# Optimization experiments

Hardware: AMD Instinct MI355X
Metric: run time of the kernel (lower is better)

The kernel has to match this reference:

```python
import jax, jax.numpy as jnp
import numpy as np

N = 8192      # number of graph nodes
C = 256       # feature_size
D = C // 2    # projection dim


def setup_inputs() -> dict:
    key = jax.random.key(0)
    ks = jax.random.split(key, 10)
    s_in = 1.0 / np.sqrt(C + 3)   # torch Linear default init scale (uniform bound)
    s_r = 1.0 / np.sqrt(D)
    return {
        "landmarks": jax.random.normal(ks[0], (1, N, 3), dtype=jnp.float32),
        "features": jax.random.normal(ks[1], (1, N, C), dtype=jnp.float32),
        # weights stored [in, out]
        "Wi": jax.random.uniform(ks[2], (C + 3, D), jnp.float32, -s_in, s_in),
        "bi": jax.random.uniform(ks[3], (D,), jnp.float32, -s_in, s_in),
        "Wj": jax.random.uniform(ks[4], (C + 3, D), jnp.float32, -s_in, s_in),
        "bj": jax.random.uniform(ks[5], (D,), jnp.float32, -s_in, s_in),
        "Wk": jax.random.uniform(ks[6], (C + 3, D), jnp.float32, -s_in, s_in),
        "bk": jax.random.uniform(ks[7], (D,), jnp.float32, -s_in, s_in),
        "Wr": jax.random.uniform(ks[8], (D, C), jnp.float32, -s_r, s_r),
        "br": jax.random.uniform(ks[9], (C,), jnp.float32, -s_r, s_r),
    }


def reference(landmarks, features, Wi, bi, Wj, bj, Wk, bk, Wr, br):
    # concat coords + features, drop the singleton batch dim: [N, C+3]
    x = jnp.concatenate([landmarks, features], axis=2)[0]
    fi = x @ Wi + bi                       # [N, D]
    fj = x @ Wj + bj                       # [N, D]
    fk = x @ Wk + bk                       # [N, D]
    att = jax.nn.sigmoid(fi @ fj.T)        # [N, N] sigmoid scores (non-softmax)
    att = att / jnp.sum(att, axis=1, keepdims=True)  # row-sum normalize
    out = (att @ fk) @ Wr + br             # [N, C] restored
    return features + out[None]            # residual, back to [1, N, C]
```

## Files before the change

kernel.cpp:

```cpp
#include <hip/hip_runtime.h>
#include <stdint.h>

#define N_NODES 8192
#define KPAD 272
#define OUTC 384

typedef __attribute__((ext_vector_type(8))) short bhalf8;
typedef __attribute__((ext_vector_type(16))) float f32x16;
typedef __attribute__((ext_vector_type(4))) float f32x4;

__device__ inline unsigned short f2bf_rne(float f) {
    unsigned u = __builtin_bit_cast(unsigned, f);
    u += 0x7FFFu + ((u >> 16) & 1u);
    return (unsigned short)(u >> 16);
}

__device__ inline bhalf8 mk8(unsigned a, unsigned b, unsigned c, unsigned d) {
    union { unsigned u[4]; bhalf8 v; } U;
    U.u[0] = a; U.u[1] = b; U.u[2] = c; U.u[3] = d;
    return U.v;
}

#define GLD_TO_LDS(gptr, lptr)                                                              \
    __builtin_amdgcn_global_load_lds((const __attribute__((address_space(1))) void*)(gptr), \
                                     (__attribute__((address_space(3))) void*)(lptr), 16, 0, 0)

__global__ void k_prep(const float* __restrict__ landmarks, const float* __restrict__ features,
                       const float* __restrict__ Wi, const float* __restrict__ bi,
                       const float* __restrict__ Wj, const float* __restrict__ bj,
                       const float* __restrict__ Wk, const float* __restrict__ bk,
                       const float* __restrict__ Wr,
                       unsigned short* __restrict__ xb, unsigned short* __restrict__ WcatT,
                       unsigned short* __restrict__ WrT, float* __restrict__ bcat) {
    int idx = blockIdx.x * 256 + threadIdx.x;
    const int XB_N = N_NODES * KPAD;
    const int WC_N = OUTC * KPAD;
    const int WR_N = 256 * 128;
    if (idx < XB_N) {
        int i = idx / KPAD, kk = idx - i * KPAD;
        float v = 0.f;
        if (kk < 256) v = features[i * 256 + kk];
        else if (kk < 259) v = landmarks[i * 3 + (kk - 256)];
        xb[idx] = f2bf_rne(v);
        return;
    }
    idx -= XB_N;
    if (idx < WC_N) {
        int n = idx / KPAD, kk = idx - n * KPAD;
        int sel = n >> 7, d = n & 127;
        const float* W = (sel == 0) ? Wi : ((sel == 1) ? Wj : Wk);
        float v = 0.f;
        if (kk < 256) v = W[(kk + 3) * 128 + d];
        else if (kk < 259) v = W[(kk - 256) * 128 + d];
        WcatT[idx] = f2bf_rne(v);
        return;
    }
    idx -= WC_N;
    if (idx < WR_N) {
        int c = idx >> 7, d = idx & 127;
        WrT[idx] = f2bf_rne(Wr[d * 256 + c]);
        return;
    }
    idx -= WR_N;
    if (idx < OUTC) {
        float v = (idx < 128) ? bi[idx] : ((idx < 256) ? bj[idx - 128] : bk[idx - 256]);
        bcat[idx] = v;
    }
}

__global__ __launch_bounds__(256) void k_proj(const unsigned short* __restrict__ xb,
                                              const unsigned short* __restrict__ WcatT,
                                              const float* __restrict__ bcat,
                                              unsigned short* __restrict__ fi,
                                              unsigned short* __restrict__ fj,
                                              unsigned short* __restrict__ fkT) {
    const int tid = threadIdx.x;
    const int w = tid >> 6, l = tid & 63, h = l >> 5, ln = l & 31;
    const int i0 = blockIdx.x * 32;
    f32x16 acc[3] = {};
#pragma unroll
    for (int s = 0; s < 17; ++s) {
        bhalf8 a = *(const bhalf8*)(xb + (size_t)(i0 + ln) * KPAD + s * 16 + h * 8);
#pragma unroll
        for (int t = 0; t < 3; ++t) {
            int n = 96 * w + 32 * t + ln;
            bhalf8 b = *(const bhalf8*)(WcatT + (size_t)n * KPAD + s * 16 + h * 8);
            acc[t] = __builtin_amdgcn_mfma_f32_32x32x16_bf16(a, b, acc[t], 0, 0, 0);
        }
    }
#pragma unroll
    for (int t = 0; t < 3; ++t) {
        int n = 96 * w + 32 * t + ln;
        int sel = n >> 7, d = n & 127;
        float bias = bcat[n];
#pragma unroll
        for (int q = 0; q < 4; ++q) {
            int ib = i0 + 8 * q + 4 * h;
            if (sel < 2) {
                unsigned short* dst = sel ? fj : fi;
#pragma unroll
                for (int r = 0; r < 4; ++r)
                    dst[(size_t)(ib + r) * 128 + d] = f2bf_rne(acc[t][4 * q + r] + bias);
            } else {
                ushort4 pk;
                pk.x = f2bf_rne(acc[t][4 * q + 0] + bias);
                pk.y = f2bf_rne(acc[t][4 * q + 1] + bias);
                pk.z = f2bf_rne(acc[t][4 * q + 2] + bias);
                pk.w = f2bf_rne(acc[t][4 * q + 3] + bias);
                *(ushort4*)(fkT + (size_t)d * N_NODES + ib) = pk;
            }
        }
    }
}

__global__ __launch_bounds__(256, 2) void k_attn(const unsigned short* __restrict__ fi,
                                                 const unsigned short* __restrict__ fj,
                                                 const unsigned short* __restrict__ fkT,
                                                 float* __restrict__ num_part,
                                                 float* __restrict__ den_part) {
    __shared__ __align__(16) char smem[65536];
    unsigned short* fj_s = (unsigned short*)smem;
    unsigned short* fk_s = (unsigned short*)(smem + 32768);
    float* bufA = (float*)smem;
    float* bufB = (float*)(smem + 17408);
    float* denb = (float*)(smem + 34816);

    const int tid = threadIdx.x;
    const int w = tid >> 6, l = tid & 63, h = l >> 5, ln = l & 31;
    const int rt = blockIdx.x & 127, jq = blockIdx.x >> 7;
    const int i0 = rt * 64;
    const int jbase = jq * 2048;

    bhalf8 bfi[2][8];
#pragma unroll
    for (int nt = 0; nt < 2; ++nt)
#pragma unroll
        for (int s = 0; s < 8; ++s)
            bfi[nt][s] = *(const bhalf8*)(fi + (size_t)(i0 + nt * 32 + ln) * 128 + s * 16 + h * 8);

    f32x16 acc[8] = {};
    float dacc0 = 0.f, dacc1 = 0.f;

    const int rsub = l >> 4;
    const int cph = l & 15;

    for (int mt = 0; mt < 16; ++mt) {
        const int j0 = jbase + mt * 128;
#pragma unroll
        for (int q = 0; q < 8; ++q) {
            int r = w * 32 + q * 4 + rsub;
            int c = cph ^ (r & 15);
            GLD_TO_LDS(fj + (size_t)(j0 + r) * 128 + c * 8, (char*)fj_s + (w * 32 + q * 4) * 256);
            GLD_TO_LDS(fkT + (size_t)r * N_NODES + j0 + c * 8, (char*)fk_s + (w * 32 + q * 4) * 256);
        }
        __syncthreads();

        f32x16 st0 = {}, st1 = {};
        const int jrow = w * 32 + ln;
#pragma unroll
        for (int s = 0; s < 8; ++s) {
            int c = (s * 2 + h) ^ (jrow & 15);
            bhalf8 af = *(const bhalf8*)((char*)fj_s + jrow * 256 + c * 16);
            st0 = __builtin_amdgcn_mfma_f32_32x32x16_bf16(af, bfi[0][s], st0, 0, 0, 0);
            st1 = __builtin_amdgcn_mfma_f32_32x32x16_bf16(af, bfi[1][s], st1, 0, 0, 0);
        }

        float sv0[16], sv1[16];
#pragma unroll
        for (int r = 0; r < 16; ++r) {
            float x0 = __builtin_amdgcn_rcpf(1.f + __builtin_amdgcn_exp2f(st0[r] * -1.44269504f));
            float x1 = __builtin_amdgcn_rcpf(1.f + __builtin_amdgcn_exp2f(st1[r] * -1.44269504f));
            dacc0 += x0; dacc1 += x1;
            sv0[r] = x0; sv1[r] = x1;
        }
        unsigned p0[8], p1[8], x0v[8], x1v[8];
#pragma unroll
        for (int q = 0; q < 8; ++q) {
            p0[q] = __builtin_amdgcn_perm(__builtin_bit_cast(unsigned, sv0[2 * q + 1]),
                                          __builtin_bit_cast(unsigned, sv0[2 * q]), 0x07060302u);
            p1[q] = __builtin_amdgcn_perm(__builtin_bit_cast(unsigned, sv1[2 * q + 1]),
                                          __builtin_bit_cast(unsigned, sv1[2 * q]), 0x07060302u);
        }
#pragma unroll
        for (int q = 0; q < 8; ++q) {
            x0v[q] = (unsigned)__shfl_xor((int)p0[q], 32, 64);
            x1v[q] = (unsigned)__shfl_xor((int)p1[q], 32, 64);
        }
        bhalf8 fb[2][2];
        if (h == 0) {
            fb[0][0] = mk8(p0[0], p0[1], x0v[0], x0v[1]);
            fb[0][1] = mk8(p0[4], p0[5], x0v[4], x0v[5]);
            fb[1][0] = mk8(p1[0], p1[1], x1v[0], x1v[1]);
            fb[1][1] = mk8(p1[4], p1[5], x1v[4], x1v[5]);
        } else {
            fb[0][0] = mk8(x0v[2], x0v[3], p0[2], p0[3]);
            fb[0][1] = mk8(x0v[6], x0v[7], p0[6], p0[7]);
            fb[1][0] = mk8(x1v[2], x1v[3], p1[2], p1[3]);
            fb[1][1] = mk8(x1v[6], x1v[7], p1[6], p1[7]);
        }
#pragma unroll
        for (int m4 = 0; m4 < 4; ++m4) {
#pragma unroll
            for (int s2 = 0; s2 < 2; ++s2) {
                int row = m4 * 32 + ln;
                int c = (w * 4 + s2 * 2 + h) ^ (row & 15);
                bhalf8 af = *(const bhalf8*)((char*)fk_s + row * 256 + c * 16);
                acc[m4 * 2 + 0] = __builtin_amdgcn_mfma_f32_32x32x16_bf16(af, fb[0][s2], acc[m4 * 2 + 0], 0, 0, 0);
                acc[m4 * 2 + 1] = __builtin_amdgcn_mfma_f32_32x32x16_bf16(af, fb[1][s2], acc[m4 * 2 + 1], 0, 0, 0);
            }
        }
        __syncthreads();
    }

    {
        float o0 = __shfl_xor(dacc0, 32, 64);
        float o1 = __shfl_xor(dacc1, 32, 64);
        dacc0 += o0; dacc1 += o1;
    }
    if (h == 0) {
        denb[w * 64 + ln] = dacc0;
        denb[w * 64 + 32 + ln] = dacc1;
    }

#pragma unroll
    for (int half = 0; half < 2; ++half) {
        __syncthreads();
        if (w < 2) {
            float* buf = w ? bufB : bufA;
#pragma unroll
            for (int m2 = 0; m2 < 2; ++m2) {
                int m4 = half * 2 + m2;
#pragma unroll
                for (int nt = 0; nt < 2; ++nt) {
                    int iloc = nt * 32 + ln;
#pragma unroll
                    for (int q = 0; q < 4; ++q) {
                        int d = m2 * 32 + 8 * q + 4 * h;
                        f32x4 v = {acc[m4 * 2 + nt][4 * q + 0], acc[m4 * 2 + nt][4 * q + 1],
                                   acc[m4 * 2 + nt][4 * q + 2], acc[m4 * 2 + nt][4 * q + 3]};
                        *(f32x4*)(buf + iloc * 68 + d) = v;
                    }
                }
            }
        }
        __syncthreads();
        if (w >= 2) {
            float* buf = (w == 3) ? bufB : bufA;
#pragma unroll
            for (int m2 = 0; m2 < 2; ++m2) {
                int m4 = half * 2 + m2;
#pragma unroll
                for (int nt = 0; nt < 2; ++nt) {
                    int iloc = nt * 32 + ln;
#pragma unroll
                    for (int q = 0; q < 4; ++q) {
                        int d = m2 * 32 + 8 * q + 4 * h;
                        f32x4 old = *(f32x4*)(buf + iloc * 68 + d);
                        f32x4 v = {acc[m4 * 2 + nt][4 * q + 0], acc[m4 * 2 + nt][4 * q + 1],
                                   acc[m4 * 2 + nt][4 * q + 2], acc[m4 * 2 + nt][4 * q + 3]};
                        *(f32x4*)(buf + iloc * 68 + d) = old + v;
                    }
                }
            }
        }
        __syncthreads();
#pragma unroll
        for (int e = 0; e < 4; ++e) {
            int v = e * 256 + tid;
            int iloc = v >> 4;
            int d4 = (v & 15) * 4;
            f32x4 s = *(f32x4*)(bufA + iloc * 68 + d4) + *(f32x4*)(bufB + iloc * 68 + d4);
            *(f32x4*)(num_part + (size_t)(jq * N_NODES + i0 + iloc) * 128 + half * 64 + d4) = s;
        }
    }
    __syncthreads();
    if (tid < 64) {
        den_part[(size_t)jq * N_NODES + i0 + tid] =
            denb[tid] + denb[64 + tid] + denb[128 + tid] + denb[192 + tid];
    }
}

__global__ void k_comb(const float* __restrict__ num_part, const float* __restrict__ den_part,
                       unsigned short* __restrict__ t) {
    int f = blockIdx.x * 256 + threadIdx.x;
    int i = f >> 5, d4 = (f & 31) * 4;
    f32x4 s = {};
    float ds = 0.f;
#pragma unroll
    for (int q = 0; q < 4; ++q) {
        s += *(const f32x4*)(num_part + (size_t)(q * N_NODES + i) * 128 + d4);
        ds += den_part[(size_t)q * N_NODES + i];
    }
    float inv = 1.0f / ds;
    ushort4 pk;
    pk.x = f2bf_rne(s.x * inv);
    pk.y = f2bf_rne(s.y * inv);
    pk.z = f2bf_rne(s.z * inv);
    pk.w = f2bf_rne(s.w * inv);
    *(ushort4*)(t + (size_t)i * 128 + d4) = pk;
}

__global__ __launch_bounds__(256) void k_out(const unsigned short* __restrict__ t,
                                             const unsigned short* __restrict__ WrT,
                                             const float* __restrict__ br,
                                             const float* __restrict__ features,
                                             float* __restrict__ out) {
    __shared__ __align__(16) char smem[65536];
    const int tid = threadIdx.x, w = tid >> 6, l = tid & 63, h = l >> 5, ln = l & 31;
    const int i0 = blockIdx.x * 32;
    {
        int rsub = l >> 4, cph = l & 15;
#pragma unroll
        for (int q = 0; q < 16; ++q) {
            int r = w * 64 + q * 4 + rsub;
            int c = cph ^ (r & 15);
            GLD_TO_LDS(WrT + (size_t)r * 128 + c * 8, (char*)smem + (w * 64 + q * 4) * 256);
        }
    }
    __syncthreads();
    f32x16 acc[2] = {};
#pragma unroll
    for (int s = 0; s < 8; ++s) {
        bhalf8 af = *(const bhalf8*)(t + (size_t)(i0 + ln) * 128 + s * 16 + h * 8);
#pragma unroll
        for (int nt = 0; nt < 2; ++nt) {
            int row = w * 64 + nt * 32 + ln;
            int c = (s * 2 + h) ^ (row & 15);
            bhalf8 bf = *(const bhalf8*)((char*)smem + row * 256 + c * 16);
            acc[nt] = __builtin_amdgcn_mfma_f32_32x32x16_bf16(af, bf, acc[nt], 0, 0, 0);
        }
    }
#pragma unroll
    for (int nt = 0; nt < 2; ++nt) {
        int cc = w * 64 + nt * 32 + ln;
        float bias = br[cc];
#pragma unroll
        for (int q = 0; q < 4; ++q) {
#pragma unroll
            for (int r = 0; r < 4; ++r) {
                int i = i0 + 8 * q + 4 * h + r;
                out[(size_t)i * 256 + cc] = acc[nt][4 * q + r] + bias + features[(size_t)i * 256 + cc];
            }
        }
    }
}

extern "C" void kernel_launch(void* const* d_in, const int* in_sizes, int n_in,
                              void* d_out, int out_size, void* d_ws, size_t ws_size,
                              hipStream_t stream) {
    const float* landmarks = (const float*)d_in[0];
    const float* features  = (const float*)d_in[1];
    const float* Wi = (const float*)d_in[2];
    const float* bi = (const float*)d_in[3];
    const float* Wj = (const float*)d_in[4];
    const float* bj = (const float*)d_in[5];
    const float* Wk = (const float*)d_in[6];
    const float* bk = (const float*)d_in[7];
    const float* Wr = (const float*)d_in[8];
    const float* br = (const float*)d_in[9];

    char* ws = (char*)d_ws;
    unsigned short* xb      = (unsigned short*)(ws + 0);
    unsigned short* WcatT   = (unsigned short*)(ws + 4456448);
    unsigned short* WrT     = (unsigned short*)(ws + 4665344);
    float*          bcat    = (float*)(ws + 4730880);
    unsigned short* fi      = (unsigned short*)(ws + 4732416);
    unsigned short* fjp     = (unsigned short*)(ws + 6829568);
    unsigned short* fkT     = (unsigned short*)(ws + 8926720);
    float*          num_part= (float*)(ws + 11023872);
    float*          den_part= (float*)(ws + 27801088);
    unsigned short* t       = (unsigned short*)(ws + 27932160);

    float* out = (float*)d_out;

    hipLaunchKernelGGL(k_prep, dim3(9242), dim3(256), 0, stream,
                       landmarks, features, Wi, bi, Wj, bj, Wk, bk, Wr, xb, WcatT, WrT, bcat);
    hipLaunchKernelGGL(k_proj, dim3(256), dim3(256), 0, stream, xb, WcatT, bcat, fi, fjp, fkT);
    hipLaunchKernelGGL(k_attn, dim3(512), dim3(256), 0, stream, fi, fjp, fkT, num_part, den_part);
    hipLaunchKernelGGL(k_comb, dim3(1024), dim3(256), 0, stream, num_part, den_part, t);
    hipLaunchKernelGGL(k_out, dim3(256), dim3(256), 0, stream, t, WrT, br, features, out);
}
```

Measured before the change: 183.5 us.

## Double-buffer attention tiles and split waves over i-halves and j-halves

Result: faster. 156.3 us (-14.8%).

```diff
diff --git a/kernel.cpp b/kernel.cpp
--- a/kernel.cpp
+++ b/kernel.cpp
@@ -119,164 +119,136 @@
                                                  float* __restrict__ num_part,
                                                  float* __restrict__ den_part) {
     __shared__ __align__(16) char smem[65536];
-    unsigned short* fj_s = (unsigned short*)smem;
-    unsigned short* fk_s = (unsigned short*)(smem + 32768);
-    float* bufA = (float*)smem;
-    float* bufB = (float*)(smem + 17408);
-    float* denb = (float*)(smem + 34816);
+    char* const fjb0 = smem;
+    char* const fkb0 = smem + 16384;
+    char* const fjb1 = smem + 32768;
+    char* const fkb1 = smem + 49152;
 
     const int tid = threadIdx.x;
     const int w = tid >> 6, l = tid & 63, h = l >> 5, ln = l & 31;
+    const int ih = w >> 1, jh = w & 1;
     const int rt = blockIdx.x & 127, jq = blockIdx.x >> 7;
     const int i0 = rt * 64;
     const int jbase = jq * 2048;
 
-    bhalf8 bfi[2][8];
-#pragma unroll
-    for (int nt = 0; nt < 2; ++nt)
-#pragma unroll
-        for (int s = 0; s < 8; ++s)
-            bfi[nt][s] = *(const bhalf8*)(fi + (size_t)(i0 + nt * 32 + ln) * 128 + s * 16 + h * 8);
-
-    f32x16 acc[8] = {};
-    float dacc0 = 0.f, dacc1 = 0.f;
-
-    const int rsub = l >> 4;
-    const int cph = l & 15;
-
-    for (int mt = 0; mt < 16; ++mt) {
-        const int j0 = jbase + mt * 128;
-#pragma unroll
-        for (int q = 0; q < 8; ++q) {
-            int r = w * 32 + q * 4 + rsub;
+    const int rsub = l >> 4, cph = l & 15;
+    const int rsub8 = l >> 3, cph8 = l & 7;
+
+    bhalf8 bfi[8];
+#pragma unroll
+    for (int s = 0; s < 8; ++s)
+        bfi[s] = *(const bhalf8*)(fi + (size_t)(i0 + ih * 32 + ln) * 128 + s * 16 + h * 8);
+
+    f32x16 acc[4] = {};
+    float dacc = 0.f;
+
+    auto STAGE = [&](char* fjd, char* fkd, int J0) {
+#pragma unroll
+        for (int q = 0; q < 4; ++q) {
+            int r = w * 16 + q * 4 + rsub;
             int c = cph ^ (r & 15);
-            GLD_TO_LDS(fj + (size_t)(j0 + r) * 128 + c * 8, (char*)fj_s + (w * 32 + q * 4) * 256);
-            GLD_TO_LDS(fkT + (size_t)r * N_NODES + j0 + c * 8, (char*)fk_s + (w * 32 + q * 4) * 256);
-        }
-        __syncthreads();
-
-        f32x16 st0 = {}, st1 = {};
-        const int jrow = w * 32 + ln;
+            GLD_TO_LDS(fj + (size_t)(J0 + r) * 128 + c * 8, fjd + (w * 16 + q * 4) * 256);
+        }
+#pragma unroll
+        for (int q = 0; q < 4; ++q) {
+            int r = w * 32 + q * 8 + rsub8;
+            int c = cph8 ^ (r & 7);
+            GLD_TO_LDS(fkT + (size_t)r * N_NODES + J0 + c * 8, fkd + (w * 32 + q * 8) * 128);
+        }
+    };
+
+    auto COMPUTE = [&](const char* fjbuf, const char* fkbuf) {
+        f32x16 st = {};
+        const int jrow = jh * 32 + ln;
 #pragma unroll
         for (int s = 0; s < 8; ++s) {
             int c = (s * 2 + h) ^ (jrow & 15);
-            bhalf8 af = *(const bhalf8*)((char*)fj_s + jrow * 256 + c * 16);
-            st0 = __builtin_amdgcn_mfma_f32_32x32x16_bf16(af, bfi[0][s], st0, 0, 0, 0);
-            st1 = __builtin_amdgcn_mfma_f32_32x32x16_bf16(af, bfi[1][s], st1, 0, 0, 0);
-        }
-
-        float sv0[16], sv1[16];
-#pragma unroll
-        for (int r = 0; r < 16; ++r) {
-            float x0 = __builtin_amdgcn_rcpf(1.f + __builtin_amdgcn_exp2f(st0[r] * -1.44269504f));
-            float x1 = __builtin_amdgcn_rcpf(1.f + __builtin_amdgcn_exp2f(st1[r] * -1.44269504f));
-            dacc0 += x0; dacc1 += x1;
-            sv0[r] = x0; sv1[r] = x1;
-        }
-        unsigned p0[8], p1[8], x0v[8], x1v[8];
+            bhalf8 af = *(const bhalf8*)(fjbuf + jrow * 256 + c * 16);
+            st = __builtin_amdgcn_mfma_f32_32x32x16_bf16(af, bfi[s], st, 0, 0, 0);
+        }
+        unsigned p[8], xw[8];
 #pragma unroll
         for (int q = 0; q < 8; ++q) {
-            p0[q] = __builtin_amdgcn_perm(__builtin_bit_cast(unsigned, sv0[2 * q + 1]),
-                                          __builtin_bit_cast(unsigned, sv0[2 * q]), 0x07060302u);
-            p1[q] = __builtin_amdgcn_perm(__builtin_bit_cast(unsigned, sv1[2 * q + 1]),
-                                          __builtin_bit_cast(unsigned, sv1[2 * q]), 0x07060302u);
-        }
-#pragma unroll
-        for (int q = 0; q < 8; ++q) {
-            x0v[q] = (unsigned)__shfl_xor((int)p0[q], 32, 64);
-            x1v[q] = (unsigned)__shfl_xor((int)p1[q], 32, 64);
-        }
-        bhalf8 fb[2][2];
+            float x0 = __builtin_amdgcn_rcpf(1.f + __builtin_amdgcn_exp2f(st[2 * q] * -1.44269504f));
+            float x1 = __builtin_amdgcn_rcpf(1.f + __builtin_amdgcn_exp2f(st[2 * q + 1] * -1.44269504f));
+            dacc += x0;
+            dacc += x1;
+            p[q] = __builtin_amdgcn_perm(__builtin_bit_cast(unsigned, x1),
+                                         __builtin_bit_cast(unsigned, x0), 0x07060302u);
+        }
+#pragma unroll
+        for (int q = 0; q < 8; ++q) xw[q] = (unsigned)__shfl_xor((int)p[q], 32, 64);
+        bhalf8 fb[2];
         if (h == 0) {
-            fb[0][0] = mk8(p0[0], p0[1], x0v[0], x0v[1]);
-            fb[0][1] = mk8(p0[4], p0[5], x0v[4], x0v[5]);
-            fb[1][0] = mk8(p1[0], p1[1], x1v[0], x1v[1]);
-            fb[1][1] = mk8(p1[4], p1[5], x1v[4], x1v[5]);
+            fb[0] = mk8(p[0], p[1], xw[0], xw[1]);
+            fb[1] = mk8(p[4], p[5], xw[4], xw[5]);
         } else {
-            fb[0][0] = mk8(x0v[2], x0v[3], p0[2], p0[3]);
-            fb[0][1] = mk8(x0v[6], x0v[7], p0[6], p0[7]);
-            fb[1][0] = mk8(x1v[2], x1v[3], p1[2], p1[3]);
-            fb[1][1] = mk8(x1v[6], x1v[7], p1[6], p1[7]);
+            fb[0] = mk8(xw[2], xw[3], p[2], p[3]);
+            fb[1] = mk8(xw[6], xw[7], p[6], p[7]);
         }
 #pragma unroll
         for (int m4 = 0; m4 < 4; ++m4) {
+            int row = m4 * 32 + ln;
 #pragma unroll
             for (int s2 = 0; s2 < 2; ++s2) {
-                int row = m4 * 32 + ln;
-                int c = (w * 4 + s2 * 2 + h) ^ (row & 15);
-                bhalf8 af = *(const bhalf8*)((char*)fk_s + row * 256 + c * 16);
-                acc[m4 * 2 + 0] = __builtin_amdgcn_mfma_f32_32x32x16_bf16(af, fb[0][s2], acc[m4 * 2 + 0], 0, 0, 0);
-                acc[m4 * 2 + 1] = __builtin_amdgcn_mfma_f32_32x32x16_bf16(af, fb[1][s2], acc[m4 * 2 + 1], 0, 0, 0);
-            }
-        }
+                int c = (jh * 4 + s2 * 2 + h) ^ (row & 7);
+                bhalf8 af = *(const bhalf8*)(fkbuf + row * 128 + c * 16);
+                acc[m4] = __builtin_amdgcn_mfma_f32_32x32x16_bf16(af, fb[s2], acc[m4], 0, 0, 0);
+            }
+        }
+    };
+
+    STAGE(fjb0, fkb0, jbase);
+    __syncthreads();
+#pragma unroll 1
+    for (int mt = 0; mt < 32; mt += 2) {
+        STAGE(fjb1, fkb1, jbase + (mt + 1) * 64);
+        COMPUTE(fjb0, fkb0);
         __syncthreads();
-    }
-
-    {
-        float o0 = __shfl_xor(dacc0, 32, 64);
-        float o1 = __shfl_xor(dacc1, 32, 64);
-        dacc0 += o0; dacc1 += o1;
-    }
-    if (h == 0) {
-        denb[w * 64 + ln] = dacc0;
-        denb[w * 64 + 32 + ln] = dacc1;
-    }
-
-#pragma unroll
-    for (int half = 0; half < 2; ++half) {
+        if (mt + 2 < 32) STAGE(fjb0, fkb0, jbase + (mt + 2) * 64);
+        COMPUTE(fjb1, fkb1);
         __syncthreads();
-        if (w < 2) {
-            float* buf = w ? bufB : bufA;
-#pragma unroll
-            for (int m2 = 0; m2 < 2; ++m2) {
-                int m4 = half * 2 + m2;
-#pragma unroll
-                for (int nt = 0; nt < 2; ++nt) {
-                    int iloc = nt * 32 + ln;
-#pragma unroll
-                    for (int q = 0; q < 4; ++q) {
-                        int d = m2 * 32 + 8 * q + 4 * h;
-                        f32x4 v = {acc[m4 * 2 + nt][4 * q + 0], acc[m4 * 2 + nt][4 * q + 1],
-                                   acc[m4 * 2 + nt][4 * q + 2], acc[m4 * 2 + nt][4 * q + 3]};
-                        *(f32x4*)(buf + iloc * 68 + d) = v;
-                    }
-                }
-            }
-        }
-        __syncthreads();
-        if (w >= 2) {
-            float* buf = (w == 3) ? bufB : bufA;
-#pragma unroll
-            for (int m2 = 0; m2 < 2; ++m2) {
-                int m4 = half * 2 + m2;
-#pragma unroll
-                for (int nt = 0; nt < 2; ++nt) {
-                    int iloc = nt * 32 + ln;
-#pragma unroll
-                    for (int q = 0; q < 4; ++q) {
-                        int d = m2 * 32 + 8 * q + 4 * h;
-                        f32x4 old = *(f32x4*)(buf + iloc * 68 + d);
-                        f32x4 v = {acc[m4 * 2 + nt][4 * q + 0], acc[m4 * 2 + nt][4 * q + 1],
-                                   acc[m4 * 2 + nt][4 * q + 2], acc[m4 * 2 + nt][4 * q + 3]};
-                        *(f32x4*)(buf + iloc * 68 + d) = old + v;
-                    }
-                }
-            }
-        }
-        __syncthreads();
-#pragma unroll
-        for (int e = 0; e < 4; ++e) {
-            int v = e * 256 + tid;
-            int iloc = v >> 4;
-            int d4 = (v & 15) * 4;
-            f32x4 s = *(f32x4*)(bufA + iloc * 68 + d4) + *(f32x4*)(bufB + iloc * 68 + d4);
-            *(f32x4*)(num_part + (size_t)(jq * N_NODES + i0 + iloc) * 128 + half * 64 + d4) = s;
-        }
+    }
+
+    dacc += __shfl_xor(dacc, 32, 64);
+    float* denb = (float*)(smem + 40960);
+    if (h == 0) denb[w * 32 + ln] = dacc;
+
+    float* buf = (float*)smem;
+    if (jh == 0) {
+#pragma unroll
+        for (int m4 = 0; m4 < 4; ++m4)
+#pragma unroll
+            for (int q = 0; q < 4; ++q) {
+                f32x4 v = {acc[m4][4 * q + 0], acc[m4][4 * q + 1],
+                           acc[m4][4 * q + 2], acc[m4][4 * q + 3]};
+                *(f32x4*)(buf + (ih * 32 + ln) * 132 + m4 * 32 + 8 * q + 4 * h) = v;
+            }
     }
     __syncthreads();
+    if (jh == 1) {
+#pragma unroll
+        for (int m4 = 0; m4 < 4; ++m4)
+#pragma unroll
+            for (int q = 0; q < 4; ++q) {
+                float* p4 = buf + (ih * 32 + ln) * 132 + m4 * 32 + 8 * q + 4 * h;
+                f32x4 old = *(f32x4*)p4;
+                f32x4 v = {acc[m4][4 * q + 0], acc[m4][4 * q + 1],
+                           acc[m4][4 * q + 2], acc[m4][4 * q + 3]};
+                *(f32x4*)p4 = old + v;
+            }
+    }
+    __syncthreads();
+#pragma unroll
+    for (int e = 0; e < 8; ++e) {
+        int v = e * 256 + tid;
+        int iloc = v >> 5, d4 = (v & 31) * 4;
+        *(f32x4*)(num_part + ((size_t)jq * N_NODES + i0 + iloc) * 128 + d4) =
+            *(const f32x4*)(buf + iloc * 132 + d4);
+    }
     if (tid < 64) {
         den_part[(size_t)jq * N_NODES + i0 + tid] =
-            denb[tid] + denb[64 + tid] + denb[128 + tid] + denb[192 + tid];
+            denb[(tid >> 5) * 64 + (tid & 31)] + denb[(tid >> 5) * 64 + 32 + (tid & 31)];
     }
 }
 
```
